# Kernel tuning notes

Hardware: AMD Instinct MI355X
Metric: run time of the kernel (lower is better)

## Reference

```python
import jax, jax.numpy as jnp
import numpy as np
from jax import lax

B, L, D = 2, 4096, 1024
H = 8
DK = D // H   # head_k_dim = 128
DV = D // H   # head_v_dim = 128
CONV_K = 4
CHUNK = 32
EPS = 1e-5


def _silu(x):
    return x * jax.nn.sigmoid(x)


def _causal_depthwise_conv_silu(x, w):
    """x: (b, l, ch); w: (ch, K). Causal depthwise conv1d followed by SiLU."""
    K = w.shape[1]
    l = x.shape[1]
    xp = jnp.pad(x, ((0, 0), (K - 1, 0), (0, 0)))
    y = sum(xp[:, i:i + l, :] * w[:, i] for i in range(K))
    return _silu(y)


def _l2norm(x):
    return x * lax.rsqrt(jnp.sum(x * x, axis=-1, keepdims=True) + 1e-12)


def _delta_rule_chunkwise(q, k, v, beta, chunk=CHUNK):
    """q,k: (b,h,l,dk); v: (b,h,l,dv); beta: (b,h,l). l % chunk == 0."""
    b, h, l, dk = q.shape
    dv = v.shape[-1]
    n = l // chunk
    q = _l2norm(q)
    k = _l2norm(k)
    v = v * beta[..., None]
    kb = k * beta[..., None]
    resh = lambda t: t.reshape(b, h, n, chunk, t.shape[-1])
    q, k, v, kb = map(resh, (q, k, v, kb))

    tri_strict = jnp.tril(jnp.ones((chunk, chunk), dtype=bool), -1)  # strictly lower
    attn = jnp.where(tri_strict, -(kb @ jnp.swapaxes(k, -1, -2)), 0.0)
    # UT transform: invert (I - strictly-lower) via forward substitution over chunk rows
    col = jnp.arange(chunk)
    for i in range(1, chunk):
        row = attn[..., i, :]                                    # (b,h,n,chunk)
        upd = jnp.einsum('bhnj,bhnjk->bhnk', row, attn)
        attn = attn.at[..., i, :].set(jnp.where(col < i, row + upd, row))
    attn = attn + jnp.eye(chunk, dtype=attn.dtype)

    u = attn @ v    # (b,h,n,chunk,dv)
    w = attn @ kb   # (b,h,n,chunk,dk)

    tri_incl = jnp.tril(jnp.ones((chunk, chunk), dtype=bool))  # incl. diagonal
    qc, kc, uc, wc = (jnp.moveaxis(t, 2, 0) for t in (q, k, u, w))

    def step(S, inp):
        qi, ki, ui, wi = inp  # each (b,h,chunk,d)
        attn_i = jnp.where(tri_incl, qi @ jnp.swapaxes(ki, -1, -2), 0.0)
        ui = ui - wi @ S
        oi = qi @ S + attn_i @ ui
        S = S + jnp.swapaxes(ki, -1, -2) @ ui
        return S, oi

    S0 = jnp.zeros((b, h, dk, dv), dtype=q.dtype)
    S, o = lax.scan(step, S0, (qc, kc, uc, wc))
    o = jnp.moveaxis(o, 0, 2).reshape(b, h, l, dv)
    return o, S


def setup_inputs() -> dict:
    key = jax.random.key(0)
    ks = jax.random.split(key, 10)
    s = 0.02
    return {
        'hidden_states': jax.random.normal(ks[0], (B, L, D), jnp.float32),
        'q_w': jax.random.normal(ks[1], (D, D), jnp.float32) * s,
        'k_w': jax.random.normal(ks[2], (D, D), jnp.float32) * s,
        'v_w': jax.random.normal(ks[3], (D, D), jnp.float32) * s,
        'conv_q_w': jax.random.normal(ks[4], (D, CONV_K), jnp.float32) * 0.3,
        'conv_k_w': jax.random.normal(ks[5], (D, CONV_K), jnp.float32) * 0.3,
        'conv_v_w': jax.random.normal(ks[6], (D, CONV_K), jnp.float32) * 0.3,
        'b_w': jax.random.normal(ks[7], (D, H), jnp.float32) * s,
        'mix_w': jax.random.normal(ks[8], (D, H), jnp.float32) * s,
        'mix_b': jnp.full((H,), -1.0, jnp.float32),      # mix_proj bias (init -1)
        'mix_bias': jnp.full((H,), -1.0, jnp.float32),   # extra learned mix bias
        'o_norm_w': jnp.ones((DV,), jnp.float32),
        'o_w': jax.random.normal(ks[9], (D, D), jnp.float32) * s,
    }


def reference(hidden_states, q_w, k_w, v_w, conv_q_w, conv_k_w, conv_v_w,
              b_w, mix_w, mix_b, mix_bias, o_norm_w, o_w):
    b, l, _ = hidden_states.shape
    # projections + causal short conv (SiLU activation, qk_activation='silu')
    q = _causal_depthwise_conv_silu(hidden_states @ q_w, conv_q_w)
    k = _causal_depthwise_conv_silu(hidden_states @ k_w, conv_k_w)
    v = _causal_depthwise_conv_silu(hidden_states @ v_w, conv_v_w)

    v_token = v.reshape(b, l, H, DV)
    q = q.reshape(b, l, H, DK)
    k = k.reshape(b, l, H, DK)

    beta = jax.nn.sigmoid(hidden_states @ b_w)  # (b,l,h)

    q_r = jnp.swapaxes(q, 1, 2)        # (b,h,l,dk)
    k_r = jnp.swapaxes(k, 1, 2)
    v_r = jnp.swapaxes(v_token, 1, 2)  # (b,h,l,dv)
    beta_r = jnp.swapaxes(beta, 1, 2)  # (b,h,l)

    o, _S = _delta_rule_chunkwise(q_r, k_r, v_r, beta_r)
    o = jnp.swapaxes(o, 1, 2)          # (b,l,h,dv)

    # bias-initialised adaptive mixing gate
    g = jax.nn.sigmoid(hidden_states @ mix_w + mix_b + mix_bias)[..., None]
    o = g * o + (1.0 - g) * v_token

    # per-head RMSNorm
    o = o * lax.rsqrt(jnp.mean(o * o, axis=-1, keepdims=True) + EPS) * o_norm_w

    o = o.reshape(b, l, H * DV) @ o_w
    return o
```

## Files before the change

kernel.cpp:

```cpp
#include <hip/hip_runtime.h>
#include <cstdint>
#include <cstddef>

typedef unsigned short u16;
typedef unsigned int u32;
typedef __attribute__((ext_vector_type(4))) u16 u16x4;
typedef __attribute__((ext_vector_type(8))) u16 u16x8;
typedef __attribute__((ext_vector_type(4))) float f32x4;
typedef __attribute__((ext_vector_type(8))) __bf16 bf16x8;

#define DEV static __device__ __forceinline__

DEV u16 f2bf(float f) {
  __bf16 h = (__bf16)f;
  return __builtin_bit_cast(u16, h);
}
DEV float bf2f(u16 s) { return __builtin_bit_cast(float, (u32)s << 16); }
DEV float sigm(float x) { return __builtin_amdgcn_rcpf(1.f + __expf(-x)); }

DEV void gl_lds16(const void* g, void* l) {
  __builtin_amdgcn_global_load_lds((const __attribute__((address_space(1))) u32*)g,
                                   (__attribute__((address_space(3))) u32*)l, 16, 0, 0);
}

constexpr int B_ = 2, L_ = 4096, H_ = 8;
constexpr int BL = B_ * L_;
constexpr int NC = L_ / 32;
constexpr int QKV_N = 3200;

constexpr int WOFF = 0;
constexpr int QOFF = 4096;
constexpr int KTOFF = 8192;
constexpr int AOFF = 12288;
constexpr int UTOFF = 13312;
constexpr int BLOB_ELEMS = 17408;

__global__ __launch_bounds__(256) void k_f32_to_bf16(const float* __restrict__ src,
                                                     u16* __restrict__ dst, int n4) {
  int i = blockIdx.x * 256 + threadIdx.x;
  if (i < n4) {
    f32x4 v = *(const f32x4*)(src + (size_t)i * 4);
    u16x4 o;
#pragma unroll
    for (int j = 0; j < 4; ++j) o[j] = f2bf(v[j]);
    *(u16x4*)(dst + (size_t)i * 4) = o;
  }
}

__global__ __launch_bounds__(256) void k_transpose_w(const float* __restrict__ s0, const float* __restrict__ s1,
                                                     const float* __restrict__ s2, const float* __restrict__ s3,
                                                     u16* __restrict__ d0, u16* __restrict__ d1,
                                                     u16* __restrict__ d2, u16* __restrict__ d3) {
  const float* src = blockIdx.z == 0 ? s0 : blockIdx.z == 1 ? s1 : blockIdx.z == 2 ? s2 : s3;
  u16* dst = blockIdx.z == 0 ? d0 : blockIdx.z == 1 ? d1 : blockIdx.z == 2 ? d2 : d3;
  __shared__ float tile[32][33];
  int k0 = blockIdx.y * 32, n0 = blockIdx.x * 32;
  int ty = threadIdx.x >> 5, tx = threadIdx.x & 31;
#pragma unroll
  for (int i = 0; i < 4; ++i)
    tile[ty + 8 * i][tx] = src[(size_t)(k0 + ty + 8 * i) * 1024 + n0 + tx];
  __syncthreads();
#pragma unroll
  for (int i = 0; i < 4; ++i) {
    int nl = ty + 8 * i;
    dst[(size_t)(n0 + nl) * 1024 + k0 + tx] = f2bf(tile[tx][nl]);
  }
}

__global__ __launch_bounds__(256) void k_pack_bg(const float* __restrict__ b_w, const float* __restrict__ mix_w,
                                                 u16* __restrict__ dst) {
  int idx = blockIdx.x * 256 + threadIdx.x;
  int r = idx >> 10, d = idx & 1023;
  float v = r < 8 ? b_w[d * 8 + r] : mix_w[d * 8 + (r - 8)];
  dst[(size_t)r * 1024 + d] = f2bf(v);
}

template<bool STORE_BF16>
__global__ __launch_bounds__(256) void gemm_bt(const u16* __restrict__ A, const u16* __restrict__ Bt,
                                               void* __restrict__ Cout, int M, int N, int K) {
  __shared__ u16 Ash[2][128 * 64];
  __shared__ u16 Bsh[2][128 * 64];
  const int tid = threadIdx.x;
  const int lane = tid & 63, w = tid >> 6;
  const int wr = w >> 1, wc = w & 1;
  const int g = lane >> 4, li = lane & 15;
  const int l7 = li & 7;
  const int nbx = gridDim.x * gridDim.y;
  const int bid = blockIdx.y * gridDim.x + blockIdx.x;
  const int wg = (bid & 7) * (nbx >> 3) + (bid >> 3);
  const int mblk = (wg / gridDim.x) * 128, nblk = (wg % gridDim.x) * 128;

  auto stage = [&](int bsel, int t) {
    int kt = t << 6;
#pragma unroll
    for (int i = 0; i < 4; ++i) {
      int unit = i * 256 + tid;
      int row = unit >> 3, pslot = unit & 7;
      int gslot = pslot ^ (row & 7);
      int gk = kt + (gslot << 3);
      gl_lds16(A + (size_t)(mblk + row) * K + gk, (char*)Ash[bsel] + unit * 16);
      gl_lds16(Bt + (size_t)(nblk + row) * K + gk, (char*)Bsh[bsel] + unit * 16);
    }
  };

  f32x4 acc[4][4];
#pragma unroll
  for (int m = 0; m < 4; ++m)
#pragma unroll
    for (int n = 0; n < 4; ++n) acc[m][n] = (f32x4){0.f, 0.f, 0.f, 0.f};

  const int nsteps = K >> 6;
  stage(0, 0);
  __syncthreads();

  for (int t = 0; t < nsteps; ++t) {
    const int cur = t & 1;
    if (t + 1 < nsteps) stage(cur ^ 1, t + 1);

#pragma unroll
    for (int kk = 0; kk < 2; ++kk) {
      const int slot = ((kk * 4 + g) ^ l7) << 3;
      bf16x8 af[4], bfr[4];
#pragma unroll
      for (int m = 0; m < 4; ++m) {
        int row = wr * 64 + m * 16 + li;
        af[m] = *(const bf16x8*)&Ash[cur][row * 64 + slot];
      }
#pragma unroll
      for (int n = 0; n < 4; ++n) {
        int row = wc * 64 + n * 16 + li;
        bfr[n] = *(const bf16x8*)&Bsh[cur][row * 64 + slot];
      }
#pragma unroll
      for (int m = 0; m < 4; ++m)
#pragma unroll
        for (int n = 0; n < 4; ++n)
          acc[m][n] = __builtin_amdgcn_mfma_f32_16x16x32_bf16(af[m], bfr[n], acc[m][n], 0, 0, 0);
    }

    __syncthreads();
  }

#pragma unroll
  for (int m = 0; m < 4; ++m)
#pragma unroll
    for (int n = 0; n < 4; ++n)
#pragma unroll
      for (int r = 0; r < 4; ++r) {
        int grow = mblk + wr * 64 + m * 16 + g * 4 + r;
        int gcol = nblk + wc * 64 + n * 16 + li;
        if constexpr (STORE_BF16)
          ((u16*)Cout)[(size_t)grow * N + gcol] = f2bf(acc[m][n][r]);
        else
          ((float*)Cout)[(size_t)grow * N + gcol] = acc[m][n][r];
      }
}

__global__ __launch_bounds__(256) void k_conv(const u16* __restrict__ qkv,
                                              const float* __restrict__ cqw, const float* __restrict__ ckw,
                                              const float* __restrict__ cvw,
                                              const float* __restrict__ mix_b, const float* __restrict__ mix_bias,
                                              u16* __restrict__ qn, u16* __restrict__ kn, u16* __restrict__ kb,
                                              u16* __restrict__ vb, u16* __restrict__ vtok,
                                              float* __restrict__ gg) {
  const int blk = blockIdx.x;
  const int bh = blk >> 7, tile = blk & 127;
  const int b = bh >> 3, h = bh & 7;
  const int t0 = tile * 32;
  const int tid = threadIdx.x;
  __shared__ u16 lq[35 * 136], lk[35 * 136], lv[35 * 136];
  __shared__ float bval[32];

#pragma unroll
  for (int it = 0; it < 7; ++it) {
    int li = it * 256 + tid;
    if (li >= 1680) break;
    int strm = li / 560;
    int rem = li - strm * 560;
    int row = rem >> 4, e8 = rem & 15;
    int l = t0 - 3 + row;
    u16* dst = strm == 0 ? lq : strm == 1 ? lk : lv;
    u16x8 val = (u16x8){0, 0, 0, 0, 0, 0, 0, 0};
    if (l >= 0)
      val = *(const u16x8*)(qkv + (size_t)(b * L_ + l) * QKV_N + strm * 1024 + h * 128 + e8 * 8);
    *(u16x8*)&dst[row * 136 + e8 * 8] = val;
  }
  if (tid < 32) {
    int gt = b * L_ + t0 + tid;
    bval[tid] = sigm(bf2f(qkv[(size_t)gt * QKV_N + 3072 + h]));
    float gz = bf2f(qkv[(size_t)gt * QKV_N + 3080 + h]) + mix_b[h] + mix_bias[h];
    gg[gt * 8 + h] = sigm(gz);
  }
  __syncthreads();

  const int tok = tid >> 3, cg = tid & 7;
  const int l = t0 + tok;
  float aq[16], ak[16], av[16];

  auto do_stream = [&](const u16* lbuf, const float* wbase, float* acc) {
    u16x8 r0[4], r1[4];
#pragma unroll
    for (int i = 0; i < 4; ++i) {
      int base = (tok + i) * 136 + cg * 16;
      r0[i] = *(const u16x8*)&lbuf[base];
      r1[i] = *(const u16x8*)&lbuf[base + 8];
    }
#pragma unroll
    for (int e = 0; e < 8; ++e) {
      f32x4 w0 = *(const f32x4*)(wbase + e * 4);
      f32x4 w1 = *(const f32x4*)(wbase + (e + 8) * 4);
      float s0 = 0.f, s1 = 0.f;
#pragma unroll
      for (int i = 0; i < 4; ++i) {
        s0 += bf2f(r0[i][e]) * w0[i];
        s1 += bf2f(r1[i][e]) * w1[i];
      }
      acc[e] = s0;
      acc[e + 8] = s1;
    }
  };
  const int chb = (h * 128 + cg * 16) * 4;
  do_stream(lq, cqw + chb, aq);
  do_stream(lk, ckw + chb, ak);
  do_stream(lv, cvw + chb, av);

  float sq2 = 0.f, sk2 = 0.f;
#pragma unroll
  for (int e = 0; e < 16; ++e) {
    aq[e] = aq[e] * sigm(aq[e]);
    ak[e] = ak[e] * sigm(ak[e]);
    av[e] = av[e] * sigm(av[e]);
    sq2 += aq[e] * aq[e];
    sk2 += ak[e] * ak[e];
  }
#pragma unroll
  for (int m = 1; m <= 4; m <<= 1) {
    sq2 += __shfl_xor(sq2, m);
    sk2 += __shfl_xor(sk2, m);
  }
  float rq = rsqrtf(sq2 + 1e-12f), rk = rsqrtf(sk2 + 1e-12f);
  float bv = bval[tok];
  size_t hoff = ((size_t)bh * L_ + l) * 128 + cg * 16;
  size_t toff = ((size_t)(b * L_ + l)) * 1024 + h * 128 + cg * 16;
#pragma unroll
  for (int part = 0; part < 2; ++part) {
    u16x8 oq, ok, okb, ovb, ovt;
#pragma unroll
    for (int e = 0; e < 8; ++e) {
      float q = aq[part * 8 + e] * rq;
      float kk = ak[part * 8 + e] * rk;
      float vv = av[part * 8 + e];
      oq[e] = f2bf(q);
      ok[e] = f2bf(kk);
      okb[e] = f2bf(kk * bv);
      ovb[e] = f2bf(vv * bv);
      ovt[e] = f2bf(vv);
    }
    *(u16x8*)(qn + hoff + part * 8) = oq;
    *(u16x8*)(kn + hoff + part * 8) = ok;
    *(u16x8*)(kb + hoff + part * 8) = okb;
    *(u16x8*)(vb + hoff + part * 8) = ovb;
    *(u16x8*)(vtok + toff + part * 8) = ovt;
  }
}

__global__ __launch_bounds__(256) void k_chunkprep(const u16* __restrict__ qn, const u16* __restrict__ kn,
                                                   const u16* __restrict__ kb, const u16* __restrict__ vb,
                                                   u16* __restrict__ blob) {
  const int blk = blockIdx.x;
  const int bh = blk >> 7, ch = blk & 127;
  const int tid = threadIdx.x;
  const int wave = tid >> 6, lane = tid & 63;
  const int g = lane >> 4, li = lane & 15;
  __shared__ u16 kbl[32 * 136], knl[32 * 136], vbl[32 * 136], qnl[32 * 136];
  __shared__ float Af[32][33];
  __shared__ float Qs[32][33];
  __shared__ float Xs[32][33];
  __shared__ float Ts[16][17];
  __shared__ u16 w_s[32 * 136];

  size_t base = ((size_t)bh * L_ + (size_t)ch * 32) * 128;
#pragma unroll
  for (int rep = 0; rep < 2; ++rep) {
    int lin = rep * 2048 + tid * 8;
    int row = lin >> 7, col = lin & 127;
    *(u16x8*)&kbl[row * 136 + col] = *(const u16x8*)(kb + base + lin);
    *(u16x8*)&knl[row * 136 + col] = *(const u16x8*)(kn + base + lin);
    *(u16x8*)&vbl[row * 136 + col] = *(const u16x8*)(vb + base + lin);
    *(u16x8*)&qnl[row * 136 + col] = *(const u16x8*)(qn + base + lin);
  }
  __syncthreads();

  u16* bp = blob + (size_t)blk * BLOB_ELEMS;

  if (wave < 2) {
    const u16* asrc = (wave == 0) ? kbl : qnl;
    bf16x8 a[2][4], bfr[2][4];
#pragma unroll
    for (int mt = 0; mt < 2; ++mt)
#pragma unroll
      for (int ks = 0; ks < 4; ++ks) {
        a[mt][ks] = *(const bf16x8*)&asrc[(mt * 16 + li) * 136 + ks * 32 + g * 8];
        bfr[mt][ks] = *(const bf16x8*)&knl[(mt * 16 + li) * 136 + ks * 32 + g * 8];
      }
    f32x4 acc[2][2];
#pragma unroll
    for (int mt = 0; mt < 2; ++mt)
#pragma unroll
      for (int nt = 0; nt < 2; ++nt) acc[mt][nt] = (f32x4){0.f, 0.f, 0.f, 0.f};
#pragma unroll
    for (int mt = 0; mt < 2; ++mt)
#pragma unroll
      for (int nt = 0; nt < 2; ++nt)
#pragma unroll
        for (int ks = 0; ks < 4; ++ks)
          acc[mt][nt] = __builtin_amdgcn_mfma_f32_16x16x32_bf16(a[mt][ks], bfr[nt][ks], acc[mt][nt], 0, 0, 0);
    if (wave == 0) {
#pragma unroll
      for (int mt = 0; mt < 2; ++mt)
#pragma unroll
        for (int nt = 0; nt < 2; ++nt)
#pragma unroll
          for (int r = 0; r < 4; ++r)
            Af[mt * 16 + g * 4 + r][nt * 16 + li] = acc[mt][nt][r];
    } else {
#pragma unroll
      for (int mt = 0; mt < 2; ++mt)
#pragma unroll
        for (int nt = 0; nt < 2; ++nt)
#pragma unroll
          for (int r = 0; r < 4; ++r) {
            int row = mt * 16 + g * 4 + r, col = nt * 16 + li;
            Qs[row][col] = (col <= row) ? acc[mt][nt][r] : 0.f;
          }
    }
  } else {
#pragma unroll
    for (int it = 0; it < 4; ++it) {
      int v8 = (tid - 128) * 4 + it;
      int f = v8 >> 6, l = v8 & 63;
      int lli = l & 15, lg = l >> 4;
      int dk = f * 16 + lli;
      u16x8 tv;
#pragma unroll
      for (int e = 0; e < 8; ++e) tv[e] = knl[(lg * 8 + e) * 136 + dk];
      *(u16x8*)(bp + KTOFF + (size_t)v8 * 8) = tv;
    }
  }
  __syncthreads();

  if (wave == 0) {
    if (lane < 32) {
      for (int i = 0; i < 32; ++i) Xs[i][lane] = (i == lane) ? 1.f : 0.f;
      int hb = lane >> 4, j = lane & 15, b0 = hb * 16;
      for (int i = j + 1; i < 16; ++i) {
        float s = 0.f;
        for (int m = j; m < i; ++m) s += Af[b0 + i][b0 + m] * Xs[b0 + m][b0 + j];
        Xs[b0 + i][b0 + j] = -s;
      }
    }
    asm volatile("s_waitcnt lgkmcnt(0)" ::: "memory");
#pragma unroll
    for (int t = 0; t < 4; ++t) {
      int idx = lane * 4 + t;
      int i = idx >> 4, j = idx & 15;
      float s = 0.f;
      for (int m = 0; m < 16; ++m) s += Af[16 + i][m] * Xs[m][j];
      Ts[i][j] = s;
    }
    asm volatile("s_waitcnt lgkmcnt(0)" ::: "memory");
#pragma unroll
    for (int t = 0; t < 4; ++t) {
      int idx = lane * 4 + t;
      int i = idx >> 4, j = idx & 15;
      float s = 0.f;
      for (int m = 0; m < 16; ++m) s += Xs[16 + i][16 + m] * Ts[m][j];
      Xs[16 + i][j] = -s;
    }
  } else if (wave == 1) {
#pragma unroll
    for (int mw = 0; mw < 2; ++mw) {
      u16x8 tv;
#pragma unroll
      for (int e = 0; e < 8; ++e) tv[e] = f2bf(Qs[mw * 16 + li][g * 8 + e]);
      *(u16x8*)(bp + AOFF + (size_t)(mw * 64 + lane) * 8) = tv;
    }
  }
  __syncthreads();

  {
    bf16x8 xa[2];
#pragma unroll
    for (int mw = 0; mw < 2; ++mw) {
      u16x8 xv;
#pragma unroll
      for (int e = 0; e < 8; ++e) xv[e] = f2bf(Xs[mw * 16 + li][g * 8 + e]);
      xa[mw] = __builtin_bit_cast(bf16x8, xv);
    }
    const u16* bsrc = (wave < 2) ? vbl : kbl;
    const int wsel = wave & 1;
#pragma unroll
    for (int s4 = 0; s4 < 4; ++s4) {
      int sg = wsel * 4 + s4;
      u16x8 bv;
#pragma unroll
      for (int e = 0; e < 8; ++e) bv[e] = bsrc[(g * 8 + e) * 136 + sg * 16 + li];
      bf16x8 bfrag = __builtin_bit_cast(bf16x8, bv);
      f32x4 a0 = (f32x4){0.f, 0.f, 0.f, 0.f};
      f32x4 a1 = (f32x4){0.f, 0.f, 0.f, 0.f};
      a0 = __builtin_amdgcn_mfma_f32_16x16x32_bf16(xa[0], bfrag, a0, 0, 0, 0);
      a1 = __builtin_amdgcn_mfma_f32_16x16x32_bf16(xa[1], bfrag, a1, 0, 0, 0);
      if (wave < 2) {
        u16x4 o0, o1;
#pragma unroll
        for (int r = 0; r < 4; ++r) { o0[r] = f2bf(a0[r]); o1[r] = f2bf(a1[r]); }
        *(u16x4*)(bp + UTOFF + (size_t)((sg * 2 + 0) * 64 + lane) * 4) = o0;
        *(u16x4*)(bp + UTOFF + (size_t)((sg * 2 + 1) * 64 + lane) * 4) = o1;
      } else {
#pragma unroll
        for (int r = 0; r < 4; ++r) {
          w_s[(0 * 16 + g * 4 + r) * 136 + sg * 16 + li] = f2bf(a0[r]);
          w_s[(1 * 16 + g * 4 + r) * 136 + sg * 16 + li] = f2bf(a1[r]);
        }
      }
    }
  }
  __syncthreads();

#pragma unroll
  for (int it = 0; it < 2; ++it) {
    int v8 = tid * 2 + it;
    int f = v8 >> 6, l = v8 & 63;
    int lli = l & 15, lg = l >> 4;
    int mw = f >> 2, ks = f & 3;
    int row = mw * 16 + lli, c0 = ks * 32 + lg * 8;
    *(u16x8*)(bp + WOFF + (size_t)v8 * 8) = *(const u16x8*)&w_s[row * 136 + c0];
    *(u16x8*)(bp + QOFF + (size_t)v8 * 8) = *(const u16x8*)&qnl[row * 136 + c0];
  }
}

struct Frags {
  bf16x8 aw[8], aq[8], akt[8], aat[2];
  u16x4 uv[2];
};

DEV void load_frags(Frags& f, const u16* __restrict__ bp, int lane, int sg) {
#pragma unroll
  for (int i = 0; i < 8; ++i)
    f.aw[i] = *(const bf16x8*)&bp[WOFF + ((size_t)(i * 64 + lane)) * 8];
#pragma unroll
  for (int mw = 0; mw < 2; ++mw)
    f.uv[mw] = *(const u16x4*)&bp[UTOFF + ((size_t)((sg * 2 + mw) * 64 + lane)) * 4];
#pragma unroll
  for (int i = 0; i < 8; ++i)
    f.aq[i] = *(const bf16x8*)&bp[QOFF + ((size_t)(i * 64 + lane)) * 8];
#pragma unroll
  for (int mw = 0; mw < 2; ++mw)
    f.aat[mw] = *(const bf16x8*)&bp[AOFF + ((size_t)(mw * 64 + lane)) * 8];
#pragma unroll
  for (int i = 0; i < 8; ++i)
    f.akt[i] = *(const bf16x8*)&bp[KTOFF + ((size_t)(i * 64 + lane)) * 8];
}

DEV void compute_chunk(const Frags& f, f32x4 (&S)[8], u16* st, u16* uft,
                       u16* __restrict__ o_out, size_t obase, int lane) {
  const int g = lane >> 4, li = lane & 15;
#pragma unroll
  for (int mi = 0; mi < 8; ++mi) {
    u16x4 sv;
#pragma unroll
    for (int r = 0; r < 4; ++r) sv[r] = f2bf(S[mi][r]);
    *(u16x4*)&st[li * 136 + mi * 16 + g * 4] = sv;
  }
  bf16x8 bS[4];
#pragma unroll
  for (int ks = 0; ks < 4; ++ks)
    bS[ks] = *(const bf16x8*)&st[li * 136 + ks * 32 + g * 8];

  f32x4 t1a[2], t1b[2];
#pragma unroll
  for (int mw = 0; mw < 2; ++mw) {
    t1a[mw] = (f32x4){0.f, 0.f, 0.f, 0.f};
    t1b[mw] = (f32x4){0.f, 0.f, 0.f, 0.f};
    t1a[mw] = __builtin_amdgcn_mfma_f32_16x16x32_bf16(f.aw[mw * 4 + 0], bS[0], t1a[mw], 0, 0, 0);
    t1b[mw] = __builtin_amdgcn_mfma_f32_16x16x32_bf16(f.aw[mw * 4 + 2], bS[2], t1b[mw], 0, 0, 0);
    t1a[mw] = __builtin_amdgcn_mfma_f32_16x16x32_bf16(f.aw[mw * 4 + 1], bS[1], t1a[mw], 0, 0, 0);
    t1b[mw] = __builtin_amdgcn_mfma_f32_16x16x32_bf16(f.aw[mw * 4 + 3], bS[3], t1b[mw], 0, 0, 0);
  }

#pragma unroll
  for (int mw = 0; mw < 2; ++mw) {
    u16x4 ufv;
#pragma unroll
    for (int r = 0; r < 4; ++r)
      ufv[r] = f2bf(bf2f(f.uv[mw][r]) - (t1a[mw][r] + t1b[mw][r]));
    *(u16x4*)&uft[li * 40 + mw * 16 + g * 4] = ufv;
  }
  bf16x8 bUF = *(const bf16x8*)&uft[li * 40 + g * 8];

  f32x4 oa[2];
  oa[0] = (f32x4){0.f, 0.f, 0.f, 0.f};
  oa[1] = (f32x4){0.f, 0.f, 0.f, 0.f};
#pragma unroll
  for (int mw = 0; mw < 2; ++mw)
#pragma unroll
    for (int ks = 0; ks < 4; ++ks)
      oa[mw] = __builtin_amdgcn_mfma_f32_16x16x32_bf16(f.aq[mw * 4 + ks], bS[ks], oa[mw], 0, 0, 0);
#pragma unroll
  for (int mw = 0; mw < 2; ++mw)
    oa[mw] = __builtin_amdgcn_mfma_f32_16x16x32_bf16(f.aat[mw], bUF, oa[mw], 0, 0, 0);

#pragma unroll
  for (int mw = 0; mw < 2; ++mw)
#pragma unroll
    for (int r = 0; r < 4; ++r)
      o_out[obase + (size_t)(mw * 16 + r) * 1024] = f2bf(oa[mw][r]);

#pragma unroll
  for (int mi = 0; mi < 8; ++mi)
    S[mi] = __builtin_amdgcn_mfma_f32_16x16x32_bf16(f.akt[mi], bUF, S[mi], 0, 0, 0);
}

__global__ __launch_bounds__(64, 1) void k_scan(const u16* __restrict__ blob, u16* __restrict__ o_out) {
  __shared__ u16 st[16 * 136];
  __shared__ u16 uft[16 * 40];
  const int bid = blockIdx.x;
  const int bh = (bid & 7) | ((bid >> 6) << 3);
  const int sg = (bid >> 3) & 7;
  const int b = bh >> 3, h = bh & 7;
  const int lane = threadIdx.x;
  const int g = lane >> 4, li = lane & 15;

  f32x4 S[8];
#pragma unroll
  for (int mi = 0; mi < 8; ++mi) S[mi] = (f32x4){0.f, 0.f, 0.f, 0.f};

  const u16* gb = blob + (size_t)bh * NC * BLOB_ELEMS;
  const size_t ob0 = ((size_t)b * L_ + g * 4) * 1024 + h * 128 + sg * 16 + li;

  Frags fa, fb;
  load_frags(fa, gb, lane, sg);
  for (int ch = 0; ch < NC - 2; ch += 2) {
    load_frags(fb, gb + (size_t)(ch + 1) * BLOB_ELEMS, lane, sg);
    compute_chunk(fa, S, st, uft, o_out, ob0 + (size_t)ch * 32 * 1024, lane);
    load_frags(fa, gb + (size_t)(ch + 2) * BLOB_ELEMS, lane, sg);
    compute_chunk(fb, S, st, uft, o_out, ob0 + (size_t)(ch + 1) * 32 * 1024, lane);
  }
  load_frags(fb, gb + (size_t)(NC - 1) * BLOB_ELEMS, lane, sg);
  compute_chunk(fa, S, st, uft, o_out, ob0 + (size_t)(NC - 2) * 32 * 1024, lane);
  compute_chunk(fb, S, st, uft, o_out, ob0 + (size_t)(NC - 1) * 32 * 1024, lane);
}

__global__ __launch_bounds__(256) void k_mixnorm(const u16* __restrict__ o_mid, const u16* __restrict__ vtok,
                                                 const float* __restrict__ g, const float* __restrict__ onw,
                                                 u16* __restrict__ omix) {
  int t = blockIdx.x, tid = threadIdx.x;
  int c = tid * 4, h = c >> 7, dk = c & 127;
  float gv = g[t * 8 + h];
  u16x4 ov = *(const u16x4*)(o_mid + (size_t)t * 1024 + c);
  u16x4 vv = *(const u16x4*)(vtok + (size_t)t * 1024 + c);
  float mx[4];
#pragma unroll
  for (int j = 0; j < 4; ++j) mx[j] = gv * bf2f(ov[j]) + (1.f - gv) * bf2f(vv[j]);
  float ss = mx[0] * mx[0] + mx[1] * mx[1] + mx[2] * mx[2] + mx[3] * mx[3];
#pragma unroll
  for (int m = 1; m <= 16; m <<= 1) ss += __shfl_xor(ss, m);
  float r = rsqrtf(ss * (1.f / 128.f) + 1e-5f);
  u16x4 oo;
#pragma unroll
  for (int j = 0; j < 4; ++j) oo[j] = f2bf(mx[j] * r * onw[dk + j]);
  *(u16x4*)(omix + (size_t)t * 1024 + c) = oo;
}

extern "C" void kernel_launch(void* const* d_in, const int* in_sizes, int n_in,
                              void* d_out, int out_size, void* d_ws, size_t ws_size,
                              hipStream_t stream) {
  const float* hidden = (const float*)d_in[0];
  const float* q_w = (const float*)d_in[1];
  const float* k_w = (const float*)d_in[2];
  const float* v_w = (const float*)d_in[3];
  const float* cqw = (const float*)d_in[4];
  const float* ckw = (const float*)d_in[5];
  const float* cvw = (const float*)d_in[6];
  const float* b_w = (const float*)d_in[7];
  const float* mix_w = (const float*)d_in[8];
  const float* mix_b = (const float*)d_in[9];
  const float* mix_bias = (const float*)d_in[10];
  const float* onw = (const float*)d_in[11];
  const float* o_w = (const float*)d_in[12];

  char* ws = (char*)d_ws;
  size_t off = 0;
  auto alloc = [&](size_t bytes) {
    char* p = ws + off;
    off += (bytes + 255) & ~(size_t)255;
    return p;
  };
  u16* hbf = (u16*)alloc(16777216);
  u16* wqkvT = (u16*)alloc((size_t)QKV_N * 1024 * 2);
  u16* woT = (u16*)alloc(2097152);
  float* gg = (float*)alloc(262144);
  u16* qn = (u16*)alloc(16777216);
  u16* kn = (u16*)alloc(16777216);
  u16* kbn = (u16*)alloc(16777216);
  u16* vbn = (u16*)alloc(16777216);
  u16* vtok = (u16*)alloc(16777216);
  u16* blob = (u16*)alloc(71303168);
  if (off > ws_size) return;

  u16* qkv = blob;
  u16* obuf = qn;

  k_f32_to_bf16<<<8192, 256, 0, stream>>>(hidden, hbf, 2097152);
  k_transpose_w<<<dim3(32, 32, 4), 256, 0, stream>>>(q_w, k_w, v_w, o_w,
                                                     wqkvT, wqkvT + 1024 * 1024,
                                                     wqkvT + 2 * 1024 * 1024, woT);
  k_pack_bg<<<64, 256, 0, stream>>>(b_w, mix_w, wqkvT + (size_t)3072 * 1024);
  gemm_bt<true><<<dim3(25, 64), 256, 0, stream>>>(hbf, wqkvT, qkv, BL, QKV_N, 1024);
  k_conv<<<2048, 256, 0, stream>>>(qkv, cqw, ckw, cvw, mix_b, mix_bias,
                                   qn, kn, kbn, vbn, vtok, gg);
  k_chunkprep<<<2048, 256, 0, stream>>>(qn, kn, kbn, vbn, blob);
  k_scan<<<128, 64, 0, stream>>>(blob, obuf);
  k_mixnorm<<<8192, 256, 0, stream>>>(obuf, vtok, gg, onw, hbf);
  gemm_bt<false><<<dim3(8, 64), 256, 0, stream>>>(hbf, woT, d_out, BL, 1024, 1024);
}
```

Before: 304.8 us.

## Load GEMM A operand directly into registers, keep only B in LDS

The bf16 GEMM no longer stages the A tile through shared memory. Each lane loads its A fragments straight from global memory into registers, double-buffered across two register sets, while B still goes through LDS via global_load_lds. Launch bounds now request two blocks per CU. The aim is to halve LDS traffic and footprint to raise occupancy. The cost is higher register pressure and less coalesced A loads, since each lane reads 16-byte pieces from different rows.

```diff
diff --git a/kernel.cpp b/kernel.cpp
--- a/kernel.cpp
+++ b/kernel.cpp
@@ -76,9 +76,8 @@
 }
 
 template<bool STORE_BF16>
-__global__ __launch_bounds__(256) void gemm_bt(const u16* __restrict__ A, const u16* __restrict__ Bt,
-                                               void* __restrict__ Cout, int M, int N, int K) {
-  __shared__ u16 Ash[2][128 * 64];
+__global__ __launch_bounds__(256, 2) void gemm_bt(const u16* __restrict__ A, const u16* __restrict__ Bt,
+                                                  void* __restrict__ Cout, int M, int N, int K) {
   __shared__ u16 Bsh[2][128 * 64];
   const int tid = threadIdx.x;
   const int lane = tid & 63, w = tid >> 6;
@@ -90,18 +89,25 @@
   const int wg = (bid & 7) * (nbx >> 3) + (bid >> 3);
   const int mblk = (wg / gridDim.x) * 128, nblk = (wg % gridDim.x) * 128;
 
-  auto stage = [&](int bsel, int t) {
+  auto stageB = [&](int bsel, int t) {
     int kt = t << 6;
 #pragma unroll
     for (int i = 0; i < 4; ++i) {
       int unit = i * 256 + tid;
       int row = unit >> 3, pslot = unit & 7;
-      int gslot = pslot ^ (row & 7);
-      int gk = kt + (gslot << 3);
-      gl_lds16(A + (size_t)(mblk + row) * K + gk, (char*)Ash[bsel] + unit * 16);
+      int gk = kt + ((pslot ^ (row & 7)) << 3);
       gl_lds16(Bt + (size_t)(nblk + row) * K + gk, (char*)Bsh[bsel] + unit * 16);
     }
   };
+  const u16* abase = A + (size_t)(mblk + wr * 64 + li) * K + g * 8;
+  auto loadA = [&](bf16x8 (&af)[8], int t) {
+    int kt = t << 6;
+#pragma unroll
+    for (int kk = 0; kk < 2; ++kk)
+#pragma unroll
+      for (int m = 0; m < 4; ++m)
+        af[kk * 4 + m] = *(const bf16x8*)(abase + (size_t)(m * 16) * K + kt + kk * 32);
+  };
 
   f32x4 acc[4][4];
 #pragma unroll
@@ -109,35 +115,36 @@
 #pragma unroll
     for (int n = 0; n < 4; ++n) acc[m][n] = (f32x4){0.f, 0.f, 0.f, 0.f};
 
-  const int nsteps = K >> 6;
-  stage(0, 0);
-  __syncthreads();
-
-  for (int t = 0; t < nsteps; ++t) {
-    const int cur = t & 1;
-    if (t + 1 < nsteps) stage(cur ^ 1, t + 1);
-
+  auto computeK = [&](const bf16x8 (&af)[8], const u16* bsh) {
 #pragma unroll
     for (int kk = 0; kk < 2; ++kk) {
       const int slot = ((kk * 4 + g) ^ l7) << 3;
-      bf16x8 af[4], bfr[4];
-#pragma unroll
-      for (int m = 0; m < 4; ++m) {
-        int row = wr * 64 + m * 16 + li;
-        af[m] = *(const bf16x8*)&Ash[cur][row * 64 + slot];
-      }
+      bf16x8 bfr[4];
 #pragma unroll
       for (int n = 0; n < 4; ++n) {
         int row = wc * 64 + n * 16 + li;
-        bfr[n] = *(const bf16x8*)&Bsh[cur][row * 64 + slot];
+        bfr[n] = *(const bf16x8*)&bsh[row * 64 + slot];
       }
 #pragma unroll
       for (int m = 0; m < 4; ++m)
 #pragma unroll
         for (int n = 0; n < 4; ++n)
-          acc[m][n] = __builtin_amdgcn_mfma_f32_16x16x32_bf16(af[m], bfr[n], acc[m][n], 0, 0, 0);
-    }
-
+          acc[m][n] = __builtin_amdgcn_mfma_f32_16x16x32_bf16(af[kk * 4 + m], bfr[n], acc[m][n], 0, 0, 0);
+    }
+  };
+
+  const int nsteps = K >> 6;
+  bf16x8 afA[8], afB[8];
+  stageB(0, 0);
+  loadA(afA, 0);
+  __syncthreads();
+
+  for (int t = 0; t < nsteps; t += 2) {
+    if (t + 1 < nsteps) { stageB(1, t + 1); loadA(afB, t + 1); }
+    computeK(afA, Bsh[0]);
+    __syncthreads();
+    if (t + 2 < nsteps) { stageB(0, t + 2); loadA(afA, t + 2); }
+    if (t + 1 < nsteps) computeK(afB, Bsh[1]);
     __syncthreads();
   }
 
```

After: 376.8 us. 1.24x slower.
